# Kernel tuning notes

Hardware: AMD Instinct MI355X
Metric: run time of the kernel (lower is better)

## Reference

```python
import jax, jax.numpy as jnp
import numpy as np

B, L, D, H, FF = 2, 2048, 1024, 16, 4096


def _xavier(key, out_d, in_d):
    lim = (6.0 / (in_d + out_d)) ** 0.5
    return jax.random.uniform(key, (out_d, in_d), jnp.float32, -lim, lim)


def setup_inputs() -> dict:
    key = jax.random.key(0)
    ks = jax.random.split(key, 7)
    x = jax.random.normal(ks[0], (B, L, D), dtype=jnp.float32)
    wq = _xavier(ks[1], D, D)
    wk = _xavier(ks[2], D, D)
    wv = _xavier(ks[3], D, D)
    wo = _xavier(ks[4], D, D)
    w1 = _xavier(ks[5], FF, D)
    w2 = _xavier(ks[6], D, FF)
    zD = jnp.zeros((D,), jnp.float32)
    return dict(x=x, wq=wq, bq=zD, wk=wk, bk=zD, wv=wv, bv=zD, wo=wo, bo=zD,
                w1=w1, b1=jnp.zeros((FF,), jnp.float32), w2=w2, b2=zD)


def _ln2d(x, eps=1e-5):
    # F.layer_norm(x, x.shape[1:]): normalize jointly over (L, D), no affine
    mu = jnp.mean(x, axis=(1, 2), keepdims=True)
    var = jnp.var(x, axis=(1, 2), keepdims=True)
    return (x - mu) * jax.lax.rsqrt(var + eps)


def reference(x, wq, bq, wk, bk, wv, bv, wo, bo, w1, b1, w2, b2):
    Bx, Lx, Dx = x.shape
    nH = H
    Dh = Dx // nH
    h = _ln2d(x)
    q = (h @ wq.T + bq).reshape(Bx, Lx, nH, Dh).transpose(0, 2, 1, 3)  # (B,H,L,Dh)
    k = (h @ wk.T + bk).reshape(Bx, Lx, nH, Dh).transpose(0, 2, 1, 3)
    v = (h @ wv.T + bv).reshape(Bx, Lx, nH, Dh).transpose(0, 2, 1, 3)
    # NOTE: faithful to source bug: scale = 1/sqrt(key.size(dim=1)) = 1/sqrt(num_heads)
    scale = 1.0 / jnp.sqrt(jnp.asarray(nH, jnp.float32))
    att = jax.nn.softmax(jnp.einsum('bhqd,bhkd->bhqk', q, k) * scale, axis=-1)
    o = jnp.einsum('bhqk,bhkd->bhqd', att, v).transpose(0, 2, 1, 3).reshape(Bx, Lx, Dx)
    o = o @ wo.T + bo
    y = _ln2d(o + x)
    ff = jax.nn.relu(y @ w1.T + b1) @ w2.T + b2
    return ff + x  # second residual adds the ORIGINAL x (as in source)
```

## Files before the change

kernel.cpp:

```cpp
#include <hip/hip_runtime.h>
#include <cstdint>
#include <cstddef>

typedef unsigned short u16;
typedef unsigned int uint;
typedef __bf16 bf16x8 __attribute__((ext_vector_type(8)));
typedef float f32x4 __attribute__((ext_vector_type(4)));

#define BATCH 2
#define SEQ 2048
#define DIM 1024
#define NH 16
#define DH 64
#define FFD 4096
#define MROWS 4096
#define PER_BATCH 2097152

__device__ __forceinline__ u16 f2b(float f) {
  uint u = __builtin_bit_cast(uint, f);
  u += 0x7FFFu + ((u >> 16) & 1u);
  return (u16)(u >> 16);
}

__device__ __forceinline__ uint pkbf2(float a, float b) {
  u16 x = __builtin_bit_cast(u16, (__bf16)a);
  u16 y = __builtin_bit_cast(u16, (__bf16)b);
  return (uint)x | ((uint)y << 16);
}

__device__ __forceinline__ int xcd_swz(int flat, int nwg) {
  return (flat & 7) * (nwg >> 3) + (flat >> 3);
}

#define GLL(gp, lp)                                                            \
  __builtin_amdgcn_global_load_lds(                                            \
      (const __attribute__((address_space(1))) void*)(gp),                     \
      (__attribute__((address_space(3))) void*)(lp), 16, 0, 0)

__global__ __launch_bounds__(256) void cvt4_kernel(const float* __restrict__ s0,
                                                   const float* __restrict__ s1,
                                                   const float* __restrict__ s2,
                                                   const float* __restrict__ s3,
                                                   u16* d0, u16* d1, u16* d2, u16* d3,
                                                   int n) {
  int t = blockIdx.y;
  const float* src = (t == 0) ? s0 : (t == 1) ? s1 : (t == 2) ? s2 : s3;
  u16* dst = (t == 0) ? d0 : (t == 1) ? d1 : (t == 2) ? d2 : d3;
  int i = (blockIdx.x * 256 + threadIdx.x) * 8;
  if (i >= n) return;
  float4 a = *(const float4*)(src + i);
  float4 b = *(const float4*)(src + i + 4);
  uint4 o;
  o.x = f2b(a.x) | ((uint)f2b(a.y) << 16);
  o.y = f2b(a.z) | ((uint)f2b(a.w) << 16);
  o.z = f2b(b.x) | ((uint)f2b(b.y) << 16);
  o.w = f2b(b.z) | ((uint)f2b(b.w) << 16);
  *(uint4*)(dst + i) = o;
}

__global__ __launch_bounds__(256) void reduce_stats_kernel(const float* __restrict__ x,
                                                           float* __restrict__ stats) {
  int b = blockIdx.y;
  const float* p = x + (size_t)b * PER_BATCH;
  float s = 0.f, ss = 0.f;
  int stride = gridDim.x * 256 * 4;
  for (int i = (blockIdx.x * 256 + threadIdx.x) * 4; i < PER_BATCH; i += stride) {
    float4 v = *(const float4*)(p + i);
    s  += (v.x + v.y) + (v.z + v.w);
    ss += (v.x * v.x + v.y * v.y) + (v.z * v.z + v.w * v.w);
  }
#pragma unroll
  for (int m = 32; m; m >>= 1) { s += __shfl_xor(s, m); ss += __shfl_xor(ss, m); }
  __shared__ float red[16];
  int w = threadIdx.x >> 6;
  if ((threadIdx.x & 63) == 0) { red[w] = s; red[8 + w] = ss; }
  __syncthreads();
  if (threadIdx.x == 0) {
    atomicAdd(&stats[b * 2],     red[0] + red[1] + red[2] + red[3]);
    atomicAdd(&stats[b * 2 + 1], red[8] + red[9] + red[10] + red[11]);
  }
}

__global__ __launch_bounds__(256) void ln_apply_kernel(const float* __restrict__ xin,
                                                       const float* __restrict__ stats,
                                                       u16* __restrict__ out) {
  int i = (blockIdx.x * 256 + threadIdx.x) * 4;
  int b = i >> 21;
  const float inv = 1.f / (float)PER_BATCH;
  float mu = stats[b * 2] * inv;
  float var = stats[b * 2 + 1] * inv - mu * mu;
  float rs = rsqrtf(var + 1e-5f);
  float4 v = *(const float4*)(xin + i);
  uint r0 = f2b((v.x - mu) * rs) | ((uint)f2b((v.y - mu) * rs) << 16);
  uint r1 = f2b((v.z - mu) * rs) | ((uint)f2b((v.w - mu) * rs) << 16);
  *(uint2*)(out + i) = make_uint2(r0, r1);
}

template <int TN, int RELU, int RESID, int OUTBF, int TRV, int DBUF>
__device__ __forceinline__ void gemm_bt_body(const u16* __restrict__ A,
                                             const u16* __restrict__ Bm,
                                             const float* __restrict__ bias,
                                             const float* __restrict__ resid,
                                             void* __restrict__ Cout,
                                             int M, int N, int K,
                                             int m0, int n0, float oscale) {
  constexpr int AI  = (TN == 128) ? 4 : 2;
  constexpr int BCH = (TN == 128) ? 4 : 2;
  constexpr int NB  = DBUF ? 2 : 1;
  __shared__ __align__(16) u16 As[NB][128 * 64];
  __shared__ __align__(16) u16 Bs[NB][TN * 64];
  const int tid = threadIdx.x;
  const int lane = tid & 63, w = tid >> 6;
  const int wr = (TN == 128) ? (w >> 1) : w;
  const int wc = (TN == 128) ? (w & 1) : 0;
  const int ln = lane & 15, qd = lane >> 4;

  f32x4 acc[AI][4] = {};

  const int lrow = lane >> 3;
  const int scl  = (lane & 7) ^ lrow;
  const u16* Ag = A  + (size_t)(m0 + w * 32 + lrow) * K + scl * 8;
  const u16* Bg = Bm + (size_t)(n0 + w * 8 * BCH + lrow) * K + scl * 8;

  const int co0 = ((qd)     ^ (ln & 7)) * 8;
  const int co1 = ((4 + qd) ^ (ln & 7)) * 8;

  auto STAGE = [&](int buf, int k0) {
#pragma unroll
    for (int r = 0; r < 4; ++r)
      GLL(Ag + (size_t)(r * 8) * K + k0, As[buf] + (w * 4 + r) * 512);
#pragma unroll
    for (int r = 0; r < BCH; ++r)
      GLL(Bg + (size_t)(r * 8) * K + k0, Bs[buf] + (w * BCH + r) * 512);
  };

  auto COMPUTE = [&](int buf) {
#pragma unroll
    for (int kk = 0; kk < 2; ++kk) {
      const int co = kk ? co1 : co0;
      bf16x8 af[AI], bf[4];
#pragma unroll
      for (int t = 0; t < AI; ++t)
        af[t] = *(const bf16x8*)&As[buf][(wr * (AI * 16) + t * 16 + ln) * 64 + co];
#pragma unroll
      for (int t = 0; t < 4; ++t)
        bf[t] = *(const bf16x8*)&Bs[buf][(wc * 64 + t * 16 + ln) * 64 + co];
#pragma unroll
      for (int i = 0; i < AI; ++i)
#pragma unroll
        for (int j = 0; j < 4; ++j)
          acc[i][j] = __builtin_amdgcn_mfma_f32_16x16x32_bf16(af[i], bf[j], acc[i][j], 0, 0, 0);
    }
  };

  if constexpr (NB == 2) {
    const int nk = K >> 6;
    STAGE(0, 0);
    for (int t = 0; t < nk; ++t) {
      const int p = t & 1;
      __syncthreads();
      if (t + 1 < nk) STAGE(1 - p, (t + 1) * 64);
      COMPUTE(p);
    }
  } else {
    for (int k0 = 0; k0 < K; k0 += 64) {
      __syncthreads();
      STAGE(0, k0);
      __syncthreads();
      COMPUTE(0);
    }
  }

#pragma unroll
  for (int i = 0; i < AI; ++i) {
    int row = m0 + wr * (AI * 16) + i * 16 + qd * 4;
#pragma unroll
    for (int j = 0; j < 4; ++j) {
      int col = n0 + wc * 64 + j * 16 + ln;
      float bv = bias[col];
      if (TRV) {
        union { uint2 u2; u16 us[4]; } pk;
#pragma unroll
        for (int r = 0; r < 4; ++r) pk.us[r] = f2b(acc[i][j][r] + bv);
        *(uint2*)&((u16*)Cout)[(size_t)col * MROWS + row] = pk.u2;
      } else {
#pragma unroll
        for (int r = 0; r < 4; ++r) {
          float v = (acc[i][j][r] + bv) * oscale;
          if (RELU) v = fmaxf(v, 0.f);
          size_t off = (size_t)(row + r) * N + col;
          if (RESID) v += resid[off];
          if (OUTBF) ((u16*)Cout)[off] = f2b(v);
          else       ((float*)Cout)[off] = v;
        }
      }
    }
  }
}

template <int TN, int RELU, int RESID, int OUTBF, int DBUF>
__global__ __launch_bounds__(256) void gemm_bt_kernel(const u16* __restrict__ A,
                                                      const u16* __restrict__ Bm,
                                                      const float* __restrict__ bias,
                                                      const float* __restrict__ resid,
                                                      void* __restrict__ Cout,
                                                      int M, int N, int K) {
  const int nx = gridDim.x;
  const int nwg = nx * gridDim.y;
  const int wid = xcd_swz(blockIdx.x + nx * blockIdx.y, nwg);
  gemm_bt_body<TN, RELU, RESID, OUTBF, 0, DBUF>(A, Bm, bias, resid, Cout, M, N, K,
                                                (wid / nx) * 128, (wid % nx) * TN, 1.0f);
}

template <int RELU>
__global__ __launch_bounds__(512, 2) void gemm256_kernel(const u16* __restrict__ A,
                                                         const u16* __restrict__ Bm,
                                                         const float* __restrict__ bias,
                                                         u16* __restrict__ Cout,
                                                         int M, int N, int K) {
  __shared__ __align__(16) u16 As[2][256 * 64];
  __shared__ __align__(16) u16 Bs[2][256 * 64];
  const int tid = threadIdx.x;
  const int lane = tid & 63, w = tid >> 6;
  const int wr = w >> 2, wc = w & 3;
  const int ln = lane & 15, qd = lane >> 4;

  const int nx = gridDim.x;
  const int nwg = nx * gridDim.y;
  const int wid = xcd_swz(blockIdx.x + nx * blockIdx.y, nwg);
  const int m0 = (wid / nx) * 256, n0 = (wid % nx) * 256;

  f32x4 acc[8][4] = {};

  const int lrow = lane >> 3;
  const int scl  = (lane & 7) ^ lrow;
  const u16* Ag = A  + (size_t)(m0 + w * 32 + lrow) * K + scl * 8;
  const u16* Bg = Bm + (size_t)(n0 + w * 32 + lrow) * K + scl * 8;

  const int co0 = ((qd)     ^ (ln & 7)) * 8;
  const int co1 = ((4 + qd) ^ (ln & 7)) * 8;

  auto STAGE = [&](int buf, int k0) {
#pragma unroll
    for (int r = 0; r < 4; ++r) {
      GLL(Ag + (size_t)(r * 8) * K + k0, As[buf] + (w * 4 + r) * 512);
      GLL(Bg + (size_t)(r * 8) * K + k0, Bs[buf] + (w * 4 + r) * 512);
    }
  };

  auto COMPUTE = [&](int buf) {
#pragma unroll
    for (int kk = 0; kk < 2; ++kk) {
      const int co = kk ? co1 : co0;
      bf16x8 af[8], bf[4];
#pragma unroll
      for (int t = 0; t < 8; ++t)
        af[t] = *(const bf16x8*)&As[buf][(wr * 128 + t * 16 + ln) * 64 + co];
#pragma unroll
      for (int t = 0; t < 4; ++t)
        bf[t] = *(const bf16x8*)&Bs[buf][(wc * 64 + t * 16 + ln) * 64 + co];
      __builtin_amdgcn_s_setprio(1);
#pragma unroll
      for (int i = 0; i < 8; ++i)
#pragma unroll
        for (int j = 0; j < 4; ++j)
          acc[i][j] = __builtin_amdgcn_mfma_f32_16x16x32_bf16(af[i], bf[j], acc[i][j], 0, 0, 0);
      __builtin_amdgcn_s_setprio(0);
    }
  };

  const int nk = K >> 6;
  STAGE(0, 0);
  for (int t = 0; t < nk; ++t) {
    const int p = t & 1;
    __syncthreads();
    if (t + 1 < nk) STAGE(1 - p, (t + 1) * 64);
    COMPUTE(p);
  }

#pragma unroll
  for (int i = 0; i < 8; ++i) {
    int row = m0 + wr * 128 + i * 16 + qd * 4;
#pragma unroll
    for (int j = 0; j < 4; ++j) {
      int col = n0 + wc * 64 + j * 16 + ln;
      float bv = bias[col];
#pragma unroll
      for (int r = 0; r < 4; ++r) {
        float v = acc[i][j][r] + bv;
        if (RELU) v = fmaxf(v, 0.f);
        Cout[(size_t)(row + r) * N + col] = f2b(v);
      }
    }
  }
}

__global__ __launch_bounds__(256) void gemm_qkv_kernel(const u16* __restrict__ A,
                                                       const u16* B0, const u16* B1, const u16* B2,
                                                       const float* c0, const float* c1, const float* c2,
                                                       u16* o0, u16* o1, u16* o2) {
  int z = blockIdx.z;
  const int wid = xcd_swz(blockIdx.x + 8 * blockIdx.y, 256);
  const int m0 = (wid >> 3) * 128, n0 = (wid & 7) * 128;
  if (z == 2) {
    gemm_bt_body<128, 0, 0, 1, 1, 0>(A, B2, c2, nullptr, o2, MROWS, DIM, DIM,
                                     m0, n0, 1.0f);
  } else {
    const u16* Bm = (z == 0) ? B0 : B1;
    const float* bias = (z == 0) ? c0 : c1;
    u16* Cout = (z == 0) ? o0 : o1;
    float sc = (z == 0) ? 0.25f : 1.0f;
    gemm_bt_body<128, 0, 0, 1, 0, 0>(A, Bm, bias, nullptr, Cout, MROWS, DIM, DIM,
                                     m0, n0, sc);
  }
}

__global__ __launch_bounds__(256, 2) void attn_kernel(const u16* __restrict__ Q,
                                                      const u16* __restrict__ Km,
                                                      const u16* __restrict__ vT,
                                                      u16* __restrict__ O) {
  __shared__ __align__(16) u16 Ks[2][64 * 64];
  __shared__ __align__(16) u16 Vt[2][64 * 64];
  __shared__ __align__(16) u16 Ps[4][32 * 64];

  const int tid = threadIdx.x, lane = tid & 63, w = tid >> 6;
  const int ln = lane & 15, qd = lane >> 4;
  const int flat = blockIdx.x + 16 * (blockIdx.y + 16 * blockIdx.z);
  const int wid = xcd_swz(flat, 512);
  const int qi = wid & 15, head = (wid >> 4) & 15, b = wid >> 8;
  const int wq0 = b * SEQ + qi * 128 + w * 32;
  const int hcol = head * DH;

  bf16x8 qf[2][2];
#pragma unroll
  for (int ti = 0; ti < 2; ++ti)
#pragma unroll
    for (int kk = 0; kk < 2; ++kk)
      qf[ti][kk] = *(const bf16x8*)&Q[(size_t)(wq0 + ti * 16 + ln) * DIM + hcol + kk * 32 + qd * 8];

  union { u16 u[8]; bf16x8 v; } oneu;
#pragma unroll
  for (int e = 0; e < 8; ++e) oneu.u[e] = 0x3F80;
  const bf16x8 vones = oneu.v;

  f32x4 accO[2][4] = {};
  f32x4 accL[2] = {};

  const int srow = lane >> 3;
  const int scl  = (lane & 7) ^ srow;
  const u16* Kg = Km + (size_t)(b * SEQ + w * 16 + srow) * DIM + hcol + scl * 8;
  const u16* Vg = vT + (size_t)(hcol + w * 16 + srow) * MROWS + b * SEQ + scl * 8;
  u16* Pw = Ps[w];
  const int swz = ln & 7;

#pragma unroll
  for (int r = 0; r < 2; ++r) {
    GLL(Kg + (size_t)(r * 8) * DIM,   &Ks[0][(w * 2 + r) * 512]);
    GLL(Vg + (size_t)(r * 8) * MROWS, &Vt[0][(w * 2 + r) * 512]);
  }

  for (int t = 0; t < SEQ / 64; ++t) {
    const int p = t & 1;
    const int kt = t * 64;
    __syncthreads();

    if (t + 1 < SEQ / 64) {
      const int kt2 = kt + 64;
#pragma unroll
      for (int r = 0; r < 2; ++r) {
        GLL(Kg + (size_t)(kt2 + r * 8) * DIM,   &Ks[1 - p][(w * 2 + r) * 512]);
        GLL(Vg + (size_t)(r * 8) * MROWS + kt2, &Vt[1 - p][(w * 2 + r) * 512]);
      }
    }

    f32x4 sacc[4][2] = {};
#pragma unroll
    for (int kk = 0; kk < 2; ++kk) {
      bf16x8 kf[4];
#pragma unroll
      for (int tj = 0; tj < 4; ++tj)
        kf[tj] = *(const bf16x8*)&Ks[p][(tj * 16 + ln) * 64 + (((kk * 4 + qd) ^ swz) * 8)];
      __builtin_amdgcn_s_setprio(1);
#pragma unroll
      for (int tj = 0; tj < 4; ++tj)
#pragma unroll
        for (int ti = 0; ti < 2; ++ti)
          sacc[tj][ti] = __builtin_amdgcn_mfma_f32_16x16x32_bf16(kf[tj], qf[ti][kk], sacc[tj][ti], 0, 0, 0);
      __builtin_amdgcn_s_setprio(0);
    }

#pragma unroll
    for (int tj = 0; tj < 4; ++tj)
#pragma unroll
      for (int ti = 0; ti < 2; ++ti) {
        uint lo = pkbf2(__expf(sacc[tj][ti][0]), __expf(sacc[tj][ti][1]));
        uint hi = pkbf2(__expf(sacc[tj][ti][2]), __expf(sacc[tj][ti][3]));
        *(uint2*)&Pw[(ti * 16 + ln) * 64 + (((2 * tj + (qd >> 1)) ^ swz) * 8) + (qd & 1) * 4] =
            make_uint2(lo, hi);
      }

#pragma unroll
    for (int kk = 0; kk < 2; ++kk) {
      bf16x8 pf[2], vf[4];
#pragma unroll
      for (int ti = 0; ti < 2; ++ti)
        pf[ti] = *(const bf16x8*)&Pw[(ti * 16 + ln) * 64 + (((kk * 4 + qd) ^ swz) * 8)];
#pragma unroll
      for (int tjv = 0; tjv < 4; ++tjv)
        vf[tjv] = *(const bf16x8*)&Vt[p][(tjv * 16 + ln) * 64 + (((kk * 4 + qd) ^ swz) * 8)];
      __builtin_amdgcn_s_setprio(1);
#pragma unroll
      for (int ti = 0; ti < 2; ++ti) {
#pragma unroll
        for (int tjv = 0; tjv < 4; ++tjv)
          accO[ti][tjv] = __builtin_amdgcn_mfma_f32_16x16x32_bf16(pf[ti], vf[tjv], accO[ti][tjv], 0, 0, 0);
        accL[ti] = __builtin_amdgcn_mfma_f32_16x16x32_bf16(pf[ti], vones, accL[ti], 0, 0, 0);
      }
      __builtin_amdgcn_s_setprio(0);
    }
  }

#pragma unroll
  for (int ti = 0; ti < 2; ++ti)
#pragma unroll
    for (int r = 0; r < 4; ++r) {
      float inv = 1.f / accL[ti][r];
#pragma unroll
      for (int tjv = 0; tjv < 4; ++tjv)
        O[(size_t)(wq0 + ti * 16 + qd * 4 + r) * DIM + hcol + tjv * 16 + ln] =
            f2b(accO[ti][tjv][r] * inv);
    }
}

extern "C" void kernel_launch(void* const* d_in, const int* in_sizes, int n_in,
                              void* d_out, int out_size, void* d_ws, size_t ws_size,
                              hipStream_t stream) {
  const float* x  = (const float*)d_in[0];
  const float* wq = (const float*)d_in[1];
  const float* bq = (const float*)d_in[2];
  const float* wk = (const float*)d_in[3];
  const float* bk = (const float*)d_in[4];
  const float* wv = (const float*)d_in[5];
  const float* bv = (const float*)d_in[6];
  const float* wo = (const float*)d_in[7];
  const float* bo = (const float*)d_in[8];
  const float* w1 = (const float*)d_in[9];
  const float* b1 = (const float*)d_in[10];
  const float* w2 = (const float*)d_in[11];
  const float* b2 = (const float*)d_in[12];
  float* out = (float*)d_out;
  char* ws = (char*)d_ws;

  const size_t MB = 1u << 20;
  u16*   h    = (u16*)(ws + 0);
  u16*   q    = (u16*)(ws + 8  * MB);
  u16*   k    = (u16*)(ws + 16 * MB);
  u16*   v    = (u16*)(ws + 24 * MB);
  u16*   o    = (u16*)(ws + 32 * MB);
  u16*   r    = (u16*)(ws + 8  * MB);
  float* ares = (float*)(ws + 40 * MB);
  u16*   wqb  = (u16*)(ws + 56 * MB);
  u16*   wkb  = (u16*)(ws + 58 * MB);
  u16*   wvb  = (u16*)(ws + 60 * MB);
  u16*   wob  = (u16*)(ws + 62 * MB);
  u16*   w1b  = (u16*)(ws + 64 * MB);
  u16*   w2b  = (u16*)(ws + 72 * MB);
  float* stats= (float*)(ws + 80 * MB);
  u16*   y    = h;

  (void)hipMemsetAsync(stats, 0, 64, stream);

  cvt4_kernel<<<dim3(512, 4),  256, 0, stream>>>(wq, wk, wv, wo, wqb, wkb, wvb, wob, DIM * DIM);
  cvt4_kernel<<<dim3(2048, 2), 256, 0, stream>>>(w1, w2, w1, w2, w1b, w2b, w1b, w2b, FFD * DIM);

  reduce_stats_kernel<<<dim3(64, 2), 256, 0, stream>>>(x, stats);
  ln_apply_kernel<<<4096, 256, 0, stream>>>(x, stats, h);

  gemm_qkv_kernel<<<dim3(8, 32, 3), 256, 0, stream>>>(h, wqb, wkb, wvb, bq, bk, bv, q, k, v);

  attn_kernel<<<dim3(16, 16, 2), 256, 0, stream>>>(q, k, v, o);

  gemm_bt_kernel<64, 0, 1, 0, 1><<<dim3(16, 32), 256, 0, stream>>>(o, wob, bo, x, ares, MROWS, DIM, DIM);

  reduce_stats_kernel<<<dim3(64, 2), 256, 0, stream>>>(ares, stats + 4);
  ln_apply_kernel<<<4096, 256, 0, stream>>>(ares, stats + 4, y);

  gemm256_kernel<1><<<dim3(16, 16), 512, 0, stream>>>(y, w1b, b1, r, MROWS, FFD, DIM);

  gemm_bt_kernel<64, 0, 1, 0, 1><<<dim3(16, 32), 256, 0, stream>>>(r, w2b, b2, x, out, MROWS, DIM, FFD);
}
```

Measured before the change: 357.6 us.

## Use split-K 256x256 GEMM with atomic accumulation for FFN down-projection

The second FFN GEMM (K=4096, N=1024) moves from the 128x64 tile kernel to the 256x256 tile kernel, with K split into 4 slices so the grid has 256 workgroups. An init kernel first writes x+b2 into the output. Each slice then atomically adds its fp32 partial sums into it. This gets larger tiles with more reuse while keeping enough blocks in flight, at the cost of an extra pass over the output and fp32 atomic traffic, and the summation order becomes nondeterministic.

```diff
diff --git a/kernel.cpp b/kernel.cpp
--- a/kernel.cpp
+++ b/kernel.cpp
@@ -96,6 +96,16 @@
   *(uint2*)(out + i) = make_uint2(r0, r1);
 }
 
+__global__ __launch_bounds__(256) void init_bias_resid_kernel(const float* __restrict__ x,
+                                                              const float* __restrict__ bias,
+                                                              float* __restrict__ out) {
+  int i = (blockIdx.x * 256 + threadIdx.x) * 4;
+  float4 v = *(const float4*)(x + i);
+  float4 b = *(const float4*)(bias + (i & (DIM - 1)));
+  v.x += b.x; v.y += b.y; v.z += b.z; v.w += b.w;
+  *(float4*)(out + i) = v;
+}
+
 template <int TN, int RELU, int RESID, int OUTBF, int TRV, int DBUF>
 __device__ __forceinline__ void gemm_bt_body(const u16* __restrict__ A,
                                              const u16* __restrict__ Bm,
@@ -212,11 +222,11 @@
                                                 (wid / nx) * 128, (wid % nx) * TN, 1.0f);
 }
 
-template <int RELU>
+template <int RELU, int ATOMIC>
 __global__ __launch_bounds__(512, 2) void gemm256_kernel(const u16* __restrict__ A,
                                                          const u16* __restrict__ Bm,
                                                          const float* __restrict__ bias,
-                                                         u16* __restrict__ Cout,
+                                                         void* __restrict__ Cout,
                                                          int M, int N, int K) {
   __shared__ __align__(16) u16 As[2][256 * 64];
   __shared__ __align__(16) u16 Bs[2][256 * 64];
@@ -225,17 +235,21 @@
   const int wr = w >> 2, wc = w & 3;
   const int ln = lane & 15, qd = lane >> 4;
 
-  const int nx = gridDim.x;
-  const int nwg = nx * gridDim.y;
-  const int wid = xcd_swz(blockIdx.x + nx * blockIdx.y, nwg);
-  const int m0 = (wid / nx) * 256, n0 = (wid % nx) * 256;
+  const int nx = gridDim.x, ny = gridDim.y, nz = gridDim.z;
+  const int ntile = nx * ny;
+  const int flat = blockIdx.x + nx * (blockIdx.y + ny * blockIdx.z);
+  const int wid = xcd_swz(flat, ntile * nz);
+  const int tile = wid % ntile, slice = wid / ntile;
+  const int m0 = (tile / nx) * 256, n0 = (tile % nx) * 256;
+  const int Ks = K / nz;
+  const int ko = slice * Ks;
 
   f32x4 acc[8][4] = {};
 
   const int lrow = lane >> 3;
   const int scl  = (lane & 7) ^ lrow;
-  const u16* Ag = A  + (size_t)(m0 + w * 32 + lrow) * K + scl * 8;
-  const u16* Bg = Bm + (size_t)(n0 + w * 32 + lrow) * K + scl * 8;
+  const u16* Ag = A  + (size_t)(m0 + w * 32 + lrow) * K + ko + scl * 8;
+  const u16* Bg = Bm + (size_t)(n0 + w * 32 + lrow) * K + ko + scl * 8;
 
   const int co0 = ((qd)     ^ (ln & 7)) * 8;
   const int co1 = ((4 + qd) ^ (ln & 7)) * 8;
@@ -269,7 +283,7 @@
     }
   };
 
-  const int nk = K >> 6;
+  const int nk = Ks >> 6;
   STAGE(0, 0);
   for (int t = 0; t < nk; ++t) {
     const int p = t & 1;
@@ -284,12 +298,18 @@
 #pragma unroll
     for (int j = 0; j < 4; ++j) {
       int col = n0 + wc * 64 + j * 16 + ln;
-      float bv = bias[col];
-#pragma unroll
-      for (int r = 0; r < 4; ++r) {
-        float v = acc[i][j][r] + bv;
-        if (RELU) v = fmaxf(v, 0.f);
-        Cout[(size_t)(row + r) * N + col] = f2b(v);
+      if (ATOMIC) {
+#pragma unroll
+        for (int r = 0; r < 4; ++r)
+          atomicAdd(&((float*)Cout)[(size_t)(row + r) * N + col], acc[i][j][r]);
+      } else {
+        float bv = bias[col];
+#pragma unroll
+        for (int r = 0; r < 4; ++r) {
+          float v = acc[i][j][r] + bv;
+          if (RELU) v = fmaxf(v, 0.f);
+          ((u16*)Cout)[(size_t)(row + r) * N + col] = f2b(v);
+        }
       }
     }
   }
@@ -485,7 +505,8 @@
   reduce_stats_kernel<<<dim3(64, 2), 256, 0, stream>>>(ares, stats + 4);
   ln_apply_kernel<<<4096, 256, 0, stream>>>(ares, stats + 4, y);
 
-  gemm256_kernel<1><<<dim3(16, 16), 512, 0, stream>>>(y, w1b, b1, r, MROWS, FFD, DIM);
-
-  gemm_bt_kernel<64, 0, 1, 0, 1><<<dim3(16, 32), 256, 0, stream>>>(r, w2b, b2, x, out, MROWS, DIM, FFD);
-}
+  gemm256_kernel<1, 0><<<dim3(16, 16), 512, 0, stream>>>(y, w1b, b1, r, MROWS, FFD, DIM);
+
+  init_bias_resid_kernel<<<4096, 256, 0, stream>>>(x, b2, out);
+  gemm256_kernel<0, 1><<<dim3(4, 16, 4), 512, 0, stream>>>(r, w2b, b2, out, MROWS, DIM, FFD);
+}
```

Result: slower. 389.4 us (+8.9%).
